# Kernel tuning notes

Measured on AMD Instinct MI355X. Metric: run time of the kernel, lower is better.

The kernel has to match this reference:

```python
import jax, jax.numpy as jnp
import numpy as np

S = 8192
Q_PARAM = 256
V_PARAM = 256
SCALE = 1.0 / np.sqrt(float(Q_PARAM)).astype(np.float32)


def setup_inputs() -> dict:
    key = jax.random.key(0)
    ks = jax.random.split(key, 12)
    init = lambda k, shape, fan_in: jax.random.uniform(k, shape, jnp.float32, -1.0, 1.0) / np.sqrt(float(fan_in))
    return {
        "query": jax.random.normal(ks[0], (S, Q_PARAM), jnp.float32),
        "key": jax.random.normal(ks[1], (S, Q_PARAM), jnp.float32),
        "value": jax.random.normal(ks[2], (S, V_PARAM), jnp.float32),
        "mask": jax.random.uniform(ks[3], (S, S), jnp.float32),
        "Wq": init(ks[4], (Q_PARAM, Q_PARAM), Q_PARAM),
        "bq": init(ks[5], (Q_PARAM,), Q_PARAM),
        "Wk": init(ks[6], (Q_PARAM, Q_PARAM), Q_PARAM),
        "bk": init(ks[7], (Q_PARAM,), Q_PARAM),
        "Wv": init(ks[8], (V_PARAM, V_PARAM), V_PARAM),
        "bv": init(ks[9], (V_PARAM,), V_PARAM),
        "Wo": init(ks[10], (V_PARAM, V_PARAM), V_PARAM),
        "bo": init(ks[11], (V_PARAM,), V_PARAM),
    }


def reference(query, key, value, mask, Wq, bq, Wk, bk, Wv, bv, Wo, bo):
    # torch nn.Linear: y = x @ W.T + b
    q = query @ Wq.T + bq          # [S, q]
    k = key @ Wk.T + bk            # [S, q]
    v = value @ Wv.T + bv          # [S, v]
    scores = q @ k.T               # [S, S]
    masked = scores * mask         # multiplicative mask BEFORE softmax
    h = jax.nn.softmax(masked * SCALE, axis=1)
    h = h @ v                      # [S, v]
    return h @ Wo.T + bo
```

## Files before the change

kernel.cpp:

```cpp
#include <hip/hip_runtime.h>


#define S 8192
#define NSPLIT 8
#define BM 128
#define BN 32
#define KSPL (S / NSPLIT)
#define NT (KSPL / BN)

typedef unsigned short ushort_t;
typedef __attribute__((ext_vector_type(8))) __bf16 bf16x8;
typedef __attribute__((ext_vector_type(4))) float f32x4;
typedef __attribute__((ext_vector_type(4))) ushort_t ushort4_t;
typedef __attribute__((ext_vector_type(8))) ushort_t ushort8_t;
typedef __attribute__((ext_vector_type(4))) unsigned uint4_t;

typedef const __attribute__((address_space(1))) unsigned int* gas_u32;
typedef __attribute__((address_space(3))) unsigned int* las_u32;

__device__ __forceinline__ ushort_t f2bf(float f) {
  unsigned u = __builtin_bit_cast(unsigned, f);
  u += 0x7FFFu + ((u >> 16) & 1u);
  return (ushort_t)(u >> 16);
}

__device__ __forceinline__ bf16x8 pack8(f32x4 a, f32x4 b) {
  ushort8_t u;
  u[0] = f2bf(a[0]); u[1] = f2bf(a[1]); u[2] = f2bf(a[2]); u[3] = f2bf(a[3]);
  u[4] = f2bf(b[0]); u[5] = f2bf(b[1]); u[6] = f2bf(b[2]); u[7] = f2bf(b[3]);
  return __builtin_bit_cast(bf16x8, u);
}

__device__ __forceinline__ unsigned cvt_pk_bf16(float lo, float hi) {
  unsigned r;
  asm("v_cvt_pk_bf16_f32 %0, %1, %2" : "=v"(r) : "v"(lo), "v"(hi));
  return r;
}

__global__ __launch_bounds__(256) void wconv_kernel(
    const float* __restrict__ w0, const float* __restrict__ w1,
    const float* __restrict__ w2, const float* __restrict__ w3,
    ushort_t* __restrict__ o0, ushort_t* __restrict__ o1,
    ushort_t* __restrict__ o2, ushort_t* __restrict__ o3) {
  const int m = blockIdx.y;
  const float* w = (m == 0) ? w0 : (m == 1) ? w1 : (m == 2) ? w2 : w3;
  ushort_t* o = (m == 0) ? o0 : (m == 1) ? o1 : (m == 2) ? o2 : o3;
  const int idx = (blockIdx.x * 256 + threadIdx.x) * 4;
  f32x4 v = *(const f32x4*)(w + idx);
  ushort4_t p;
  p[0] = f2bf(v[0]); p[1] = f2bf(v[1]); p[2] = f2bf(v[2]); p[3] = f2bf(v[3]);
  *(ushort4_t*)(o + idx) = p;
}

__global__ __launch_bounds__(256) void qkv_kernel(
    const float* __restrict__ query, const float* __restrict__ key,
    const float* __restrict__ value,
    const ushort_t* __restrict__ Wqb, const ushort_t* __restrict__ Wkb,
    const ushort_t* __restrict__ Wvb,
    const float* __restrict__ bq, const float* __restrict__ bk,
    const float* __restrict__ bv,
    ushort_t* __restrict__ qo, ushort_t* __restrict__ ko,
    ushort_t* __restrict__ vto) {
  __shared__ __align__(16) ushort_t tb[64 * 68];
  const int z = blockIdx.z;
  const float* inp = (z == 0) ? query : (z == 1) ? key : value;
  const ushort_t* Wb = (z == 0) ? Wqb : (z == 1) ? Wkb : Wvb;
  const float* bias = (z == 0) ? bq : (z == 1) ? bk : bv;

  const int tid = threadIdx.x;
  const int lane = tid & 63;
  const int w = tid >> 6;
  const int lr = lane & 15, lg = lane >> 4;
  const int brow0 = blockIdx.x * 64;
  const int row0 = brow0 + w * 16;
  const int col0 = blockIdx.y * 64;

  f32x4 acc[4] = {};
  const int arow = row0 + lr;
  const int kb = lg * 8;

  bf16x8 af[8];
#pragma unroll
  for (int ks = 0; ks < 8; ++ks) {
    const float* ap = inp + (size_t)arow * 256 + ks * 32 + kb;
    af[ks] = pack8(*(const f32x4*)ap, *(const f32x4*)(ap + 4));
  }
#pragma unroll
  for (int ks = 0; ks < 8; ++ks) {
#pragma unroll
    for (int n = 0; n < 4; ++n) {
      bf16x8 bb = *(const bf16x8*)(Wb + (size_t)(col0 + 16 * n + lr) * 256 + ks * 32 + kb);
      acc[n] = __builtin_amdgcn_mfma_f32_16x16x32_bf16(af[ks], bb, acc[n], 0, 0, 0);
    }
  }

  if (z < 2) {
    ushort_t* o = z ? ko : qo;
#pragma unroll
    for (int n = 0; n < 4; ++n) {
      const int col = col0 + 16 * n + lr;
      const float bv_ = bias[col];
      const int rbase = row0 + lg * 4;
#pragma unroll
      for (int r = 0; r < 4; ++r)
        o[(size_t)(rbase + r) * 256 + col] = f2bf(acc[n][r] + bv_);
    }
  } else {
#pragma unroll
    for (int n = 0; n < 4; ++n) {
      const int col = col0 + 16 * n + lr;
      const float bv_ = bias[col];
      const int cl = 16 * n + lr;
      const int rowl = w * 16 + lg * 4;
      ushort4_t pk;
#pragma unroll
      for (int r = 0; r < 4; ++r) pk[r] = f2bf(acc[n][r] + bv_);
      *(ushort4_t*)&tb[cl * 68 + rowl] = pk;
    }
    __syncthreads();
#pragma unroll
    for (int i = 0; i < 4; ++i) {
      int chunk = i * 256 + tid;
      int c = chunk >> 4;
      int off = (chunk & 15) * 4;
      ushort4_t v0 = *(const ushort4_t*)&tb[c * 68 + off];
      *(ushort4_t*)(vto + (size_t)(col0 + c) * S + brow0 + off) = v0;
    }
  }
}

__global__ __launch_bounds__(256) void oproj_kernel(const ushort_t* __restrict__ inp,
                                                    const ushort_t* __restrict__ Wb,
                                                    const float* __restrict__ bias,
                                                    float* __restrict__ outp) {
  const int tid = threadIdx.x;
  const int lane = tid & 63;
  const int w = tid >> 6;
  const int lr = lane & 15, lg = lane >> 4;
  const int row0 = blockIdx.x * 64 + w * 16;
  const int col0 = blockIdx.y * 64;

  f32x4 acc[4] = {};
  const int arow = row0 + lr;
  const int kb = lg * 8;
#pragma unroll
  for (int ks = 0; ks < 8; ++ks) {
    bf16x8 a = *(const bf16x8*)(inp + (size_t)arow * 256 + ks * 32 + kb);
#pragma unroll
    for (int n = 0; n < 4; ++n) {
      bf16x8 bb = *(const bf16x8*)(Wb + (size_t)(col0 + 16 * n + lr) * 256 + ks * 32 + kb);
      acc[n] = __builtin_amdgcn_mfma_f32_16x16x32_bf16(a, bb, acc[n], 0, 0, 0);
    }
  }
#pragma unroll
  for (int n = 0; n < 4; ++n) {
    const int col = col0 + 16 * n + lr;
    const float bv = bias[col];
    const int rbase = row0 + lg * 4;
#pragma unroll
    for (int r = 0; r < 4; ++r)
      outp[(size_t)(rbase + r) * 256 + col] = acc[n][r] + bv;
  }
}

__global__ __launch_bounds__(256, 2) void flash_kernel(
    const ushort_t* __restrict__ qg, const ushort_t* __restrict__ kbm,
    const ushort_t* __restrict__ vtb, const float* __restrict__ mask,
    float* __restrict__ Opart, float* __restrict__ lpart) {
  __shared__ __align__(16) ushort_t kt[2][BN * 256];
  __shared__ __align__(16) ushort_t vt[2][256 * BN];

  const int tid = threadIdx.x;
  const int lane = tid & 63;
  const int w = tid >> 6;
  const int lr = lane & 15, lg = lane >> 4;
  const int b = blockIdx.x;
  const int split = b & 7;
  const int qx = b >> 3;
  const int kvbase = split * KSPL;
  const int qrow0 = qx * BM + w * 32;

  bf16x8 qf[2][8];
#pragma unroll
  for (int qb = 0; qb < 2; ++qb)
#pragma unroll
    for (int ks = 0; ks < 8; ++ks)
      qf[qb][ks] = *(const bf16x8*)(qg + (size_t)(qrow0 + qb * 16 + lr) * 256 + ks * 32 + lg * 8);

  const float* mrow[2];
#pragma unroll
  for (int qb = 0; qb < 2; ++qb)
    mrow[qb] = mask + (size_t)(qrow0 + qb * 16 + lr) * S + lg * 4;

  f32x4 oacc[2][16] = {};
  float lsum[2] = {0.f, 0.f};
  const int vt_swz = ((lg ^ (lr & 3)) << 4);

  auto stage = [&](int bi, int kv0) {
#pragma unroll
    for (int it = 0; it < 4; ++it) {
      int chunk = it * 256 + (w << 6) + lane;
      int r = chunk >> 5;
      int c = (chunk & 31) ^ (r & 7);
      const ushort_t* src = kbm + (size_t)(kv0 + r) * 256 + c * 8;
      __builtin_amdgcn_global_load_lds((gas_u32)src,
                                       (las_u32)(&kt[bi][0] + it * 2048 + w * 512), 16, 0, 0);
    }
#pragma unroll
    for (int it = 0; it < 4; ++it) {
      int chunk = it * 256 + (w << 6) + lane;
      int r = chunk >> 2;
      int c = (chunk & 3) ^ (r & 3);
      const ushort_t* src = vtb + (size_t)r * S + kv0 + c * 8;
      __builtin_amdgcn_global_load_lds((gas_u32)src,
                                       (las_u32)(&vt[bi][0] + it * 2048 + w * 512), 16, 0, 0);
    }
  };

  f32x4 mcur[2][2];
  auto ld_mask = [&](int kv0) {
#pragma unroll
    for (int qb = 0; qb < 2; ++qb)
#pragma unroll
      for (int kb = 0; kb < 2; ++kb)
        mcur[qb][kb] = __builtin_nontemporal_load((const f32x4*)(mrow[qb] + kv0 + kb * 16));
  };

  stage(0, kvbase);
  ld_mask(kvbase);
  asm volatile("s_waitcnt vmcnt(4)" ::: "memory");
  __builtin_amdgcn_s_barrier();
  __builtin_amdgcn_sched_barrier(0);

  for (int t = 0; t < NT; ++t) {
    const int cur = t & 1;
    const int kvn = kvbase + ((t + 1 < NT) ? (t + 1) : t) * BN;

    stage(cur ^ 1, kvn);

    f32x4 sacc[2][2] = {};
    __builtin_amdgcn_s_setprio(1);
#pragma unroll
    for (int ks = 0; ks < 8; ++ks)
#pragma unroll
      for (int kb = 0; kb < 2; ++kb) {
        int addr = ((kb * 16 + lr) << 9) + ((((ks << 2) + lg) ^ (lr & 7)) << 4);
        bf16x8 kf = *(const bf16x8*)((const char*)&kt[cur][0] + addr);
        sacc[0][kb] = __builtin_amdgcn_mfma_f32_16x16x32_bf16(kf, qf[0][ks], sacc[0][kb], 0, 0, 0);
        sacc[1][kb] = __builtin_amdgcn_mfma_f32_16x16x32_bf16(kf, qf[1][ks], sacc[1][kb], 0, 0, 0);
      }
    __builtin_amdgcn_s_setprio(0);

    unsigned pw[2][2][2];
#pragma unroll
    for (int qb = 0; qb < 2; ++qb) {
      float p[8];
#pragma unroll
      for (int kb = 0; kb < 2; ++kb)
#pragma unroll
        for (int r = 0; r < 4; ++r) {
          float pv = __builtin_amdgcn_exp2f(sacc[qb][kb][r] * (mcur[qb][kb][r] * 0.09016844005556021f));
          p[kb * 4 + r] = pv;
          lsum[qb] += pv;
        }
      pw[qb][0][0] = cvt_pk_bf16(p[0], p[1]);
      pw[qb][0][1] = cvt_pk_bf16(p[2], p[3]);
      pw[qb][1][0] = cvt_pk_bf16(p[4], p[5]);
      pw[qb][1][1] = cvt_pk_bf16(p[6], p[7]);
    }

    ld_mask(kvn);

    bf16x8 pfrag[2];
#pragma unroll
    for (int qb = 0; qb < 2; ++qb) {
      unsigned a0 = pw[qb][0][0], a1 = pw[qb][0][1];
      unsigned b0 = pw[qb][1][0], b1 = pw[qb][1][1];
      asm("v_permlane32_swap_b32 %0, %1" : "+v"(a0), "+v"(b0));
      asm("v_permlane16_swap_b32 %0, %1" : "+v"(a0), "+v"(b0));
      asm("v_permlane32_swap_b32 %0, %1" : "+v"(a1), "+v"(b1));
      asm("v_permlane16_swap_b32 %0, %1" : "+v"(a1), "+v"(b1));
      uint4_t u = {a0, a1, b0, b1};
      pfrag[qb] = __builtin_bit_cast(bf16x8, u);
    }

    __builtin_amdgcn_s_setprio(1);
#pragma unroll
    for (int nd = 0; nd < 16; ++nd) {
      bf16x8 va = *(const bf16x8*)((const char*)&vt[cur][0] + nd * 1024 + lr * 64 + vt_swz);
      oacc[0][nd] = __builtin_amdgcn_mfma_f32_16x16x32_bf16(va, pfrag[0], oacc[0][nd], 0, 0, 0);
      oacc[1][nd] = __builtin_amdgcn_mfma_f32_16x16x32_bf16(va, pfrag[1], oacc[1][nd], 0, 0, 0);
    }
    __builtin_amdgcn_s_setprio(0);

    asm volatile("s_waitcnt vmcnt(4)" ::: "memory");
    __builtin_amdgcn_s_barrier();
    __builtin_amdgcn_sched_barrier(0);
  }

#pragma unroll
  for (int qb = 0; qb < 2; ++qb) {
    float v = lsum[qb];
    v += __shfl_xor(v, 16);
    v += __shfl_xor(v, 32);
    if (lane < 16)
      lpart[(size_t)split * S + qrow0 + qb * 16 + lr] = v;
#pragma unroll
    for (int nd = 0; nd < 16; ++nd)
      *(f32x4*)(Opart + ((size_t)split * S + qrow0 + qb * 16 + lr) * 256 + nd * 16 + lg * 4) = oacc[qb][nd];
  }
}

__global__ __launch_bounds__(256) void combine_kernel(const float* __restrict__ Opart,
                                                      const float* __restrict__ lpart,
                                                      ushort_t* __restrict__ hb) {
  const size_t idx = ((size_t)blockIdx.x * 256 + threadIdx.x) * 4;
  const int row = (int)(idx >> 8);
  float L = 0.f;
  f32x4 acc = {};
#pragma unroll
  for (int s2 = 0; s2 < NSPLIT; ++s2) {
    L += lpart[(size_t)s2 * S + row];
    f32x4 v = *(const f32x4*)(Opart + (size_t)s2 * S * 256 + idx);
    acc[0] += v[0]; acc[1] += v[1]; acc[2] += v[2]; acc[3] += v[3];
  }
  const float inv = 1.0f / L;
  ushort4_t p;
  p[0] = f2bf(acc[0] * inv); p[1] = f2bf(acc[1] * inv);
  p[2] = f2bf(acc[2] * inv); p[3] = f2bf(acc[3] * inv);
  *(ushort4_t*)(hb + idx) = p;
}

extern "C" void kernel_launch(void* const* d_in, const int* in_sizes, int n_in,
                              void* d_out, int out_size, void* d_ws, size_t ws_size,
                              hipStream_t stream) {
  const float* query = (const float*)d_in[0];
  const float* key   = (const float*)d_in[1];
  const float* value = (const float*)d_in[2];
  const float* mask  = (const float*)d_in[3];
  const float* Wq = (const float*)d_in[4];
  const float* bq = (const float*)d_in[5];
  const float* Wk = (const float*)d_in[6];
  const float* bk = (const float*)d_in[7];
  const float* Wv = (const float*)d_in[8];
  const float* bv = (const float*)d_in[9];
  const float* Wo = (const float*)d_in[10];
  const float* bo = (const float*)d_in[11];

  char* ws = (char*)d_ws;
  ushort_t* qb  = (ushort_t*)(ws);
  ushort_t* kb  = (ushort_t*)(ws + ((size_t)4  << 20));
  ushort_t* vtb = (ushort_t*)(ws + ((size_t)8  << 20));
  ushort_t* hb  = (ushort_t*)(ws + ((size_t)12 << 20));
  ushort_t* Wqb = (ushort_t*)(ws + ((size_t)16 << 20));
  ushort_t* Wkb = (ushort_t*)(ws + ((size_t)16 << 20) + (128u << 10));
  ushort_t* Wvb = (ushort_t*)(ws + ((size_t)16 << 20) + (256u << 10));
  ushort_t* Wob = (ushort_t*)(ws + ((size_t)16 << 20) + (384u << 10));
  float* lpart  = (float*)(ws + ((size_t)16 << 20) + (512u << 10));
  float* Opart  = (float*)(ws + ((size_t)17 << 20));

  wconv_kernel<<<dim3(64, 4), 256, 0, stream>>>(Wq, Wk, Wv, Wo, Wqb, Wkb, Wvb, Wob);

  qkv_kernel<<<dim3(S / 64, 4, 3), 256, 0, stream>>>(query, key, value,
                                                     Wqb, Wkb, Wvb, bq, bk, bv,
                                                     qb, kb, vtb);

  flash_kernel<<<dim3(512), 256, 0, stream>>>(qb, kb, vtb, mask, Opart, lpart);

  combine_kernel<<<dim3(S * 256 / 1024), 256, 0, stream>>>(Opart, lpart, hb);

  oproj_kernel<<<dim3(S / 64, 4), 256, 0, stream>>>(hb, Wob, bo, (float*)d_out);
}
```

Baseline: 226.6 us.

## Software-pipeline PV matmul one tile behind QK with triple-buffered V

```diff
diff --git a/kernel.cpp b/kernel.cpp
--- a/kernel.cpp
+++ b/kernel.cpp
@@ -168,7 +168,7 @@
     const ushort_t* __restrict__ vtb, const float* __restrict__ mask,
     float* __restrict__ Opart, float* __restrict__ lpart) {
   __shared__ __align__(16) ushort_t kt[2][BN * 256];
-  __shared__ __align__(16) ushort_t vt[2][256 * BN];
+  __shared__ __align__(16) ushort_t vt[3][256 * BN];
 
   const int tid = threadIdx.x;
   const int lane = tid & 63;
@@ -196,7 +196,14 @@
   float lsum[2] = {0.f, 0.f};
   const int vt_swz = ((lg ^ (lr & 3)) << 4);
 
-  auto stage = [&](int bi, int kv0) {
+  bf16x8 pfrag[2];
+  {
+    uint4_t z = {0u, 0u, 0u, 0u};
+    pfrag[0] = __builtin_bit_cast(bf16x8, z);
+    pfrag[1] = __builtin_bit_cast(bf16x8, z);
+  }
+
+  auto stage_k = [&](int bi, int kv0) {
 #pragma unroll
     for (int it = 0; it < 4; ++it) {
       int chunk = it * 256 + (w << 6) + lane;
@@ -206,6 +213,8 @@
       __builtin_amdgcn_global_load_lds((gas_u32)src,
                                        (las_u32)(&kt[bi][0] + it * 2048 + w * 512), 16, 0, 0);
     }
+  };
+  auto stage_v = [&](int bi, int kv0) {
 #pragma unroll
     for (int it = 0; it < 4; ++it) {
       int chunk = it * 256 + (w << 6) + lane;
@@ -226,26 +235,42 @@
         mcur[qb][kb] = __builtin_nontemporal_load((const f32x4*)(mrow[qb] + kv0 + kb * 16));
   };
 
-  stage(0, kvbase);
+  stage_k(0, kvbase);
+  stage_v(0, kvbase);
+  stage_v(2, kvbase);
+  __builtin_amdgcn_sched_barrier(0);
   ld_mask(kvbase);
   asm volatile("s_waitcnt vmcnt(4)" ::: "memory");
   __builtin_amdgcn_s_barrier();
   __builtin_amdgcn_sched_barrier(0);
 
+  int v_rd = 2, v_cu = 0, v_st = 1;
+
+#pragma unroll 1
   for (int t = 0; t < NT; ++t) {
-    const int cur = t & 1;
-    const int kvn = kvbase + ((t + 1 < NT) ? (t + 1) : t) * BN;
-
-    stage(cur ^ 1, kvn);
+    const int kcur = t & 1;
+    const int kvn = kvbase + ((t + 1 < NT) ? (t + 1) : 0) * BN;
+
+    stage_k(kcur ^ 1, kvn);
+    stage_v(v_st, kvn);
+    __builtin_amdgcn_sched_barrier(0);
+
+    const char* vbase = (const char*)&vt[0][0] + v_rd * 16384;
+    __builtin_amdgcn_s_setprio(1);
+#pragma unroll
+    for (int nd = 0; nd < 16; ++nd) {
+      bf16x8 va = *(const bf16x8*)(vbase + nd * 1024 + lr * 64 + vt_swz);
+      oacc[0][nd] = __builtin_amdgcn_mfma_f32_16x16x32_bf16(va, pfrag[0], oacc[0][nd], 0, 0, 0);
+      oacc[1][nd] = __builtin_amdgcn_mfma_f32_16x16x32_bf16(va, pfrag[1], oacc[1][nd], 0, 0, 0);
+    }
 
     f32x4 sacc[2][2] = {};
-    __builtin_amdgcn_s_setprio(1);
 #pragma unroll
     for (int ks = 0; ks < 8; ++ks)
 #pragma unroll
       for (int kb = 0; kb < 2; ++kb) {
         int addr = ((kb * 16 + lr) << 9) + ((((ks << 2) + lg) ^ (lr & 7)) << 4);
-        bf16x8 kf = *(const bf16x8*)((const char*)&kt[cur][0] + addr);
+        bf16x8 kf = *(const bf16x8*)((const char*)&kt[kcur][0] + addr);
         sacc[0][kb] = __builtin_amdgcn_mfma_f32_16x16x32_bf16(kf, qf[0][ks], sacc[0][kb], 0, 0, 0);
         sacc[1][kb] = __builtin_amdgcn_mfma_f32_16x16x32_bf16(kf, qf[1][ks], sacc[1][kb], 0, 0, 0);
       }
@@ -271,7 +296,6 @@
 
     ld_mask(kvn);
 
-    bf16x8 pfrag[2];
 #pragma unroll
     for (int qb = 0; qb < 2; ++qb) {
       unsigned a0 = pw[qb][0][0], a1 = pw[qb][0][1];
@@ -284,18 +308,23 @@
       pfrag[qb] = __builtin_bit_cast(bf16x8, u);
     }
 
-    __builtin_amdgcn_s_setprio(1);
-#pragma unroll
-    for (int nd = 0; nd < 16; ++nd) {
-      bf16x8 va = *(const bf16x8*)((const char*)&vt[cur][0] + nd * 1024 + lr * 64 + vt_swz);
-      oacc[0][nd] = __builtin_amdgcn_mfma_f32_16x16x32_bf16(va, pfrag[0], oacc[0][nd], 0, 0, 0);
-      oacc[1][nd] = __builtin_amdgcn_mfma_f32_16x16x32_bf16(va, pfrag[1], oacc[1][nd], 0, 0, 0);
-    }
-    __builtin_amdgcn_s_setprio(0);
-
     asm volatile("s_waitcnt vmcnt(4)" ::: "memory");
     __builtin_amdgcn_s_barrier();
     __builtin_amdgcn_sched_barrier(0);
+
+    int tmp = v_rd; v_rd = v_cu; v_cu = v_st; v_st = tmp;
+  }
+
+  {
+    const char* vbase = (const char*)&vt[0][0] + v_rd * 16384;
+    __builtin_amdgcn_s_setprio(1);
+#pragma unroll
+    for (int nd = 0; nd < 16; ++nd) {
+      bf16x8 va = *(const bf16x8*)(vbase + nd * 1024 + lr * 64 + vt_swz);
+      oacc[0][nd] = __builtin_amdgcn_mfma_f32_16x16x32_bf16(va, pfrag[0], oacc[0][nd], 0, 0, 0);
+      oacc[1][nd] = __builtin_amdgcn_mfma_f32_16x16x32_bf16(va, pfrag[1], oacc[1][nd], 0, 0, 0);
+    }
+    __builtin_amdgcn_s_setprio(0);
   }
 
 #pragma unroll
```

After: 237.5 us. 1.05x slower.

## Use 8 waves per flash block with 16 query rows each instead of 32

Applied to the files above, without the earlier changes.

```diff
diff --git a/kernel.cpp b/kernel.cpp
--- a/kernel.cpp
+++ b/kernel.cpp
@@ -163,7 +163,7 @@
   }
 }
 
-__global__ __launch_bounds__(256, 2) void flash_kernel(
+__global__ __launch_bounds__(512, 1) void flash_kernel(
     const ushort_t* __restrict__ qg, const ushort_t* __restrict__ kbm,
     const ushort_t* __restrict__ vtb, const float* __restrict__ mask,
     float* __restrict__ Opart, float* __restrict__ lpart) {
@@ -178,67 +178,54 @@
   const int split = b & 7;
   const int qx = b >> 3;
   const int kvbase = split * KSPL;
-  const int qrow0 = qx * BM + w * 32;
-
-  bf16x8 qf[2][8];
-#pragma unroll
-  for (int qb = 0; qb < 2; ++qb)
-#pragma unroll
-    for (int ks = 0; ks < 8; ++ks)
-      qf[qb][ks] = *(const bf16x8*)(qg + (size_t)(qrow0 + qb * 16 + lr) * 256 + ks * 32 + lg * 8);
-
-  const float* mrow[2];
-#pragma unroll
-  for (int qb = 0; qb < 2; ++qb)
-    mrow[qb] = mask + (size_t)(qrow0 + qb * 16 + lr) * S + lg * 4;
-
-  f32x4 oacc[2][16] = {};
-  float lsum[2] = {0.f, 0.f};
-  const int vt_swz = ((lg ^ (lr & 3)) << 4);
+  const int qrow0 = qx * BM + w * 16;
+
+  bf16x8 qf[8];
+#pragma unroll
+  for (int ks = 0; ks < 8; ++ks)
+    qf[ks] = *(const bf16x8*)(qg + (size_t)(qrow0 + lr) * 256 + ks * 32 + lg * 8);
+
+  const float* mrow = mask + (size_t)(qrow0 + lr) * S + lg * 4;
+
+  f32x4 oacc[16] = {};
+  float lsum = 0.f;
+  const int vt_swz = ((lg ^ ((lr >> 1) & 3)) << 4);
 
   auto stage = [&](int bi, int kv0) {
 #pragma unroll
-    for (int it = 0; it < 4; ++it) {
-      int chunk = it * 256 + (w << 6) + lane;
+    for (int it = 0; it < 2; ++it) {
+      int chunk = it * 512 + tid;
       int r = chunk >> 5;
       int c = (chunk & 31) ^ (r & 7);
       const ushort_t* src = kbm + (size_t)(kv0 + r) * 256 + c * 8;
       __builtin_amdgcn_global_load_lds((gas_u32)src,
-                                       (las_u32)(&kt[bi][0] + it * 2048 + w * 512), 16, 0, 0);
-    }
-#pragma unroll
-    for (int it = 0; it < 4; ++it) {
-      int chunk = it * 256 + (w << 6) + lane;
+                                       (las_u32)(&kt[bi][0] + chunk * 8), 16, 0, 0);
+    }
+#pragma unroll
+    for (int it = 0; it < 2; ++it) {
+      int chunk = it * 512 + tid;
       int r = chunk >> 2;
-      int c = (chunk & 3) ^ (r & 3);
+      int c = (chunk & 3) ^ ((r >> 1) & 3);
       const ushort_t* src = vtb + (size_t)r * S + kv0 + c * 8;
       __builtin_amdgcn_global_load_lds((gas_u32)src,
-                                       (las_u32)(&vt[bi][0] + it * 2048 + w * 512), 16, 0, 0);
+                                       (las_u32)(&vt[bi][0] + chunk * 8), 16, 0, 0);
     }
   };
 
-  f32x4 mcur[2][2];
-  auto ld_mask = [&](int kv0) {
-#pragma unroll
-    for (int qb = 0; qb < 2; ++qb)
-#pragma unroll
-      for (int kb = 0; kb < 2; ++kb)
-        mcur[qb][kb] = __builtin_nontemporal_load((const f32x4*)(mrow[qb] + kv0 + kb * 16));
-  };
-
   stage(0, kvbase);
-  ld_mask(kvbase);
-  asm volatile("s_waitcnt vmcnt(4)" ::: "memory");
+  asm volatile("s_waitcnt vmcnt(0)" ::: "memory");
   __builtin_amdgcn_s_barrier();
   __builtin_amdgcn_sched_barrier(0);
 
   for (int t = 0; t < NT; ++t) {
     const int cur = t & 1;
+    const int kv0 = kvbase + t * BN;
     const int kvn = kvbase + ((t + 1 < NT) ? (t + 1) : t) * BN;
 
     stage(cur ^ 1, kvn);
-
-    f32x4 sacc[2][2] = {};
+    __builtin_amdgcn_sched_barrier(0);
+
+    f32x4 sacc[2] = {};
     __builtin_amdgcn_s_setprio(1);
 #pragma unroll
     for (int ks = 0; ks < 8; ++ks)
@@ -246,69 +233,56 @@
       for (int kb = 0; kb < 2; ++kb) {
         int addr = ((kb * 16 + lr) << 9) + ((((ks << 2) + lg) ^ (lr & 7)) << 4);
         bf16x8 kf = *(const bf16x8*)((const char*)&kt[cur][0] + addr);
-        sacc[0][kb] = __builtin_amdgcn_mfma_f32_16x16x32_bf16(kf, qf[0][ks], sacc[0][kb], 0, 0, 0);
-        sacc[1][kb] = __builtin_amdgcn_mfma_f32_16x16x32_bf16(kf, qf[1][ks], sacc[1][kb], 0, 0, 0);
+        sacc[kb] = __builtin_amdgcn_mfma_f32_16x16x32_bf16(kf, qf[ks], sacc[kb], 0, 0, 0);
       }
     __builtin_amdgcn_s_setprio(0);
 
-    unsigned pw[2][2][2];
-#pragma unroll
-    for (int qb = 0; qb < 2; ++qb) {
-      float p[8];
-#pragma unroll
-      for (int kb = 0; kb < 2; ++kb)
-#pragma unroll
-        for (int r = 0; r < 4; ++r) {
-          float pv = __builtin_amdgcn_exp2f(sacc[qb][kb][r] * (mcur[qb][kb][r] * 0.09016844005556021f));
-          p[kb * 4 + r] = pv;
-          lsum[qb] += pv;
-        }
-      pw[qb][0][0] = cvt_pk_bf16(p[0], p[1]);
-      pw[qb][0][1] = cvt_pk_bf16(p[2], p[3]);
-      pw[qb][1][0] = cvt_pk_bf16(p[4], p[5]);
-      pw[qb][1][1] = cvt_pk_bf16(p[6], p[7]);
-    }
-
-    ld_mask(kvn);
-
-    bf16x8 pfrag[2];
-#pragma unroll
-    for (int qb = 0; qb < 2; ++qb) {
-      unsigned a0 = pw[qb][0][0], a1 = pw[qb][0][1];
-      unsigned b0 = pw[qb][1][0], b1 = pw[qb][1][1];
-      asm("v_permlane32_swap_b32 %0, %1" : "+v"(a0), "+v"(b0));
-      asm("v_permlane16_swap_b32 %0, %1" : "+v"(a0), "+v"(b0));
-      asm("v_permlane32_swap_b32 %0, %1" : "+v"(a1), "+v"(b1));
-      asm("v_permlane16_swap_b32 %0, %1" : "+v"(a1), "+v"(b1));
-      uint4_t u = {a0, a1, b0, b1};
-      pfrag[qb] = __builtin_bit_cast(bf16x8, u);
-    }
+    float p[8];
+#pragma unroll
+    for (int kb = 0; kb < 2; ++kb) {
+      f32x4 mv = __builtin_nontemporal_load((const f32x4*)(mrow + kv0 + kb * 16));
+#pragma unroll
+      for (int r = 0; r < 4; ++r) {
+        float pv = __builtin_amdgcn_exp2f(sacc[kb][r] * (mv[r] * 0.09016844005556021f));
+        p[kb * 4 + r] = pv;
+        lsum += pv;
+      }
+    }
+    unsigned pw0 = cvt_pk_bf16(p[0], p[1]);
+    unsigned pw1 = cvt_pk_bf16(p[2], p[3]);
+    unsigned pw2 = cvt_pk_bf16(p[4], p[5]);
+    unsigned pw3 = cvt_pk_bf16(p[6], p[7]);
+
+    asm("v_permlane32_swap_b32 %0, %1" : "+v"(pw0), "+v"(pw2));
+    asm("v_permlane16_swap_b32 %0, %1" : "+v"(pw0), "+v"(pw2));
+    asm("v_permlane32_swap_b32 %0, %1" : "+v"(pw1), "+v"(pw3));
+    asm("v_permlane16_swap_b32 %0, %1" : "+v"(pw1), "+v"(pw3));
+    uint4_t u = {pw0, pw1, pw2, pw3};
+    bf16x8 pfrag = __builtin_bit_cast(bf16x8, u);
 
     __builtin_amdgcn_s_setprio(1);
 #pragma unroll
     for (int nd = 0; nd < 16; ++nd) {
       bf16x8 va = *(const bf16x8*)((const char*)&vt[cur][0] + nd * 1024 + lr * 64 + vt_swz);
-      oacc[0][nd] = __builtin_amdgcn_mfma_f32_16x16x32_bf16(va, pfrag[0], oacc[0][nd], 0, 0, 0);
-      oacc[1][nd] = __builtin_amdgcn_mfma_f32_16x16x32_bf16(va, pfrag[1], oacc[1][nd], 0, 0, 0);
+      oacc[nd] = __builtin_amdgcn_mfma_f32_16x16x32_bf16(va, pfrag, oacc[nd], 0, 0, 0);
     }
     __builtin_amdgcn_s_setprio(0);
 
-    asm volatile("s_waitcnt vmcnt(4)" ::: "memory");
+    asm volatile("s_waitcnt vmcnt(0)" ::: "memory");
     __builtin_amdgcn_s_barrier();
     __builtin_amdgcn_sched_barrier(0);
   }
 
-#pragma unroll
-  for (int qb = 0; qb < 2; ++qb) {
-    float v = lsum[qb];
+  {
+    float v = lsum;
     v += __shfl_xor(v, 16);
     v += __shfl_xor(v, 32);
     if (lane < 16)
-      lpart[(size_t)split * S + qrow0 + qb * 16 + lr] = v;
-#pragma unroll
-    for (int nd = 0; nd < 16; ++nd)
-      *(f32x4*)(Opart + ((size_t)split * S + qrow0 + qb * 16 + lr) * 256 + nd * 16 + lg * 4) = oacc[qb][nd];
-  }
+      lpart[(size_t)split * S + qrow0 + lr] = v;
+  }
+#pragma unroll
+  for (int nd = 0; nd < 16; ++nd)
+    *(f32x4*)(Opart + ((size_t)split * S + qrow0 + lr) * 256 + nd * 16 + lg * 4) = oacc[nd];
 }
 
 __global__ __launch_bounds__(256) void combine_kernel(const float* __restrict__ Opart,
@@ -365,7 +339,7 @@
                                                      Wqb, Wkb, Wvb, bq, bk, bv,
                                                      qb, kb, vtb);
 
-  flash_kernel<<<dim3(512), 256, 0, stream>>>(qb, kb, vtb, mask, Opart, lpart);
+  flash_kernel<<<dim3(512), 512, 0, stream>>>(qb, kb, vtb, mask, Opart, lpart);
 
   combine_kernel<<<dim3(S * 256 / 1024), 256, 0, stream>>>(Opart, lpart, hb);
 
```

New measurement: 231.0 us. No clear change (+1.9%).

## Load K and V fragments directly from global memory instead of LDS staging

Applied to the files above, without the earlier changes.

```diff
diff --git a/kernel.cpp b/kernel.cpp
--- a/kernel.cpp
+++ b/kernel.cpp
@@ -7,6 +7,7 @@
 #define BN 32
 #define KSPL (S / NSPLIT)
 #define NT (KSPL / BN)
+#define VSTRIDE 8224
 
 typedef unsigned short ushort_t;
 typedef __attribute__((ext_vector_type(8))) __bf16 bf16x8;
@@ -14,9 +15,6 @@
 typedef __attribute__((ext_vector_type(4))) ushort_t ushort4_t;
 typedef __attribute__((ext_vector_type(8))) ushort_t ushort8_t;
 typedef __attribute__((ext_vector_type(4))) unsigned uint4_t;
-
-typedef const __attribute__((address_space(1))) unsigned int* gas_u32;
-typedef __attribute__((address_space(3))) unsigned int* las_u32;
 
 __device__ __forceinline__ ushort_t f2bf(float f) {
   unsigned u = __builtin_bit_cast(unsigned, f);
@@ -124,7 +122,7 @@
       int c = chunk >> 4;
       int off = (chunk & 15) * 4;
       ushort4_t v0 = *(const ushort4_t*)&tb[c * 68 + off];
-      *(ushort4_t*)(vto + (size_t)(col0 + c) * S + brow0 + off) = v0;
+      *(ushort4_t*)(vto + (size_t)(col0 + c) * VSTRIDE + brow0 + off) = v0;
     }
   }
 }
@@ -163,13 +161,10 @@
   }
 }
 
-__global__ __launch_bounds__(256, 2) void flash_kernel(
+__global__ __launch_bounds__(256, 1) void flash_kernel(
     const ushort_t* __restrict__ qg, const ushort_t* __restrict__ kbm,
     const ushort_t* __restrict__ vtb, const float* __restrict__ mask,
     float* __restrict__ Opart, float* __restrict__ lpart) {
-  __shared__ __align__(16) ushort_t kt[2][BN * 256];
-  __shared__ __align__(16) ushort_t vt[2][256 * BN];
-
   const int tid = threadIdx.x;
   const int lane = tid & 63;
   const int w = tid >> 6;
@@ -194,64 +189,39 @@
 
   f32x4 oacc[2][16] = {};
   float lsum[2] = {0.f, 0.f};
-  const int vt_swz = ((lg ^ (lr & 3)) << 4);
-
-  auto stage = [&](int bi, int kv0) {
-#pragma unroll
-    for (int it = 0; it < 4; ++it) {
-      int chunk = it * 256 + (w << 6) + lane;
-      int r = chunk >> 5;
-      int c = (chunk & 31) ^ (r & 7);
-      const ushort_t* src = kbm + (size_t)(kv0 + r) * 256 + c * 8;
-      __builtin_amdgcn_global_load_lds((gas_u32)src,
-                                       (las_u32)(&kt[bi][0] + it * 2048 + w * 512), 16, 0, 0);
-    }
-#pragma unroll
-    for (int it = 0; it < 4; ++it) {
-      int chunk = it * 256 + (w << 6) + lane;
-      int r = chunk >> 2;
-      int c = (chunk & 3) ^ (r & 3);
-      const ushort_t* src = vtb + (size_t)r * S + kv0 + c * 8;
-      __builtin_amdgcn_global_load_lds((gas_u32)src,
-                                       (las_u32)(&vt[bi][0] + it * 2048 + w * 512), 16, 0, 0);
-    }
-  };
 
   f32x4 mcur[2][2];
-  auto ld_mask = [&](int kv0) {
-#pragma unroll
-    for (int qb = 0; qb < 2; ++qb)
-#pragma unroll
-      for (int kb = 0; kb < 2; ++kb)
-        mcur[qb][kb] = __builtin_nontemporal_load((const f32x4*)(mrow[qb] + kv0 + kb * 16));
-  };
-
-  stage(0, kvbase);
-  ld_mask(kvbase);
-  asm volatile("s_waitcnt vmcnt(4)" ::: "memory");
-  __builtin_amdgcn_s_barrier();
-  __builtin_amdgcn_sched_barrier(0);
-
+#pragma unroll
+  for (int qb = 0; qb < 2; ++qb)
+#pragma unroll
+    for (int kb = 0; kb < 2; ++kb)
+      mcur[qb][kb] = __builtin_nontemporal_load((const f32x4*)(mrow[qb] + kvbase + kb * 16));
+
+#pragma unroll 1
   for (int t = 0; t < NT; ++t) {
-    const int cur = t & 1;
+    const int kv0 = kvbase + t * BN;
     const int kvn = kvbase + ((t + 1 < NT) ? (t + 1) : t) * BN;
 
-    stage(cur ^ 1, kvn);
+    bf16x8 vfA[8];
+#pragma unroll
+    for (int nd = 0; nd < 8; ++nd)
+      vfA[nd] = *(const bf16x8*)(vtb + (size_t)(nd * 16 + lr) * VSTRIDE + kv0 + lg * 8);
 
     f32x4 sacc[2][2] = {};
     __builtin_amdgcn_s_setprio(1);
 #pragma unroll
-    for (int ks = 0; ks < 8; ++ks)
-#pragma unroll
-      for (int kb = 0; kb < 2; ++kb) {
-        int addr = ((kb * 16 + lr) << 9) + ((((ks << 2) + lg) ^ (lr & 7)) << 4);
-        bf16x8 kf = *(const bf16x8*)((const char*)&kt[cur][0] + addr);
-        sacc[0][kb] = __builtin_amdgcn_mfma_f32_16x16x32_bf16(kf, qf[0][ks], sacc[0][kb], 0, 0, 0);
-        sacc[1][kb] = __builtin_amdgcn_mfma_f32_16x16x32_bf16(kf, qf[1][ks], sacc[1][kb], 0, 0, 0);
-      }
+    for (int ks = 0; ks < 8; ++ks) {
+      const size_t koff = (size_t)(kv0 + lr) * 256 + ks * 32 + lg * 8;
+      bf16x8 kf0 = *(const bf16x8*)(kbm + koff);
+      bf16x8 kf1 = *(const bf16x8*)(kbm + koff + 16 * 256);
+      sacc[0][0] = __builtin_amdgcn_mfma_f32_16x16x32_bf16(kf0, qf[0][ks], sacc[0][0], 0, 0, 0);
+      sacc[1][0] = __builtin_amdgcn_mfma_f32_16x16x32_bf16(kf0, qf[1][ks], sacc[1][0], 0, 0, 0);
+      sacc[0][1] = __builtin_amdgcn_mfma_f32_16x16x32_bf16(kf1, qf[0][ks], sacc[0][1], 0, 0, 0);
+      sacc[1][1] = __builtin_amdgcn_mfma_f32_16x16x32_bf16(kf1, qf[1][ks], sacc[1][1], 0, 0, 0);
+    }
     __builtin_amdgcn_s_setprio(0);
 
-    unsigned pw[2][2][2];
+    unsigned pw[2][4];
 #pragma unroll
     for (int qb = 0; qb < 2; ++qb) {
       float p[8];
@@ -263,19 +233,23 @@
           p[kb * 4 + r] = pv;
           lsum[qb] += pv;
         }
-      pw[qb][0][0] = cvt_pk_bf16(p[0], p[1]);
-      pw[qb][0][1] = cvt_pk_bf16(p[2], p[3]);
-      pw[qb][1][0] = cvt_pk_bf16(p[4], p[5]);
-      pw[qb][1][1] = cvt_pk_bf16(p[6], p[7]);
-    }
-
-    ld_mask(kvn);
+      pw[qb][0] = cvt_pk_bf16(p[0], p[1]);
+      pw[qb][1] = cvt_pk_bf16(p[2], p[3]);
+      pw[qb][2] = cvt_pk_bf16(p[4], p[5]);
+      pw[qb][3] = cvt_pk_bf16(p[6], p[7]);
+    }
+
+#pragma unroll
+    for (int qb = 0; qb < 2; ++qb)
+#pragma unroll
+      for (int kb = 0; kb < 2; ++kb)
+        mcur[qb][kb] = __builtin_nontemporal_load((const f32x4*)(mrow[qb] + kvn + kb * 16));
 
     bf16x8 pfrag[2];
 #pragma unroll
     for (int qb = 0; qb < 2; ++qb) {
-      unsigned a0 = pw[qb][0][0], a1 = pw[qb][0][1];
-      unsigned b0 = pw[qb][1][0], b1 = pw[qb][1][1];
+      unsigned a0 = pw[qb][0], a1 = pw[qb][1];
+      unsigned b0 = pw[qb][2], b1 = pw[qb][3];
       asm("v_permlane32_swap_b32 %0, %1" : "+v"(a0), "+v"(b0));
       asm("v_permlane16_swap_b32 %0, %1" : "+v"(a0), "+v"(b0));
       asm("v_permlane32_swap_b32 %0, %1" : "+v"(a1), "+v"(b1));
@@ -284,18 +258,23 @@
       pfrag[qb] = __builtin_bit_cast(bf16x8, u);
     }
 
+    bf16x8 vfB[8];
+#pragma unroll
+    for (int nd = 0; nd < 8; ++nd)
+      vfB[nd] = *(const bf16x8*)(vtb + (size_t)((nd + 8) * 16 + lr) * VSTRIDE + kv0 + lg * 8);
+
     __builtin_amdgcn_s_setprio(1);
 #pragma unroll
-    for (int nd = 0; nd < 16; ++nd) {
-      bf16x8 va = *(const bf16x8*)((const char*)&vt[cur][0] + nd * 1024 + lr * 64 + vt_swz);
-      oacc[0][nd] = __builtin_amdgcn_mfma_f32_16x16x32_bf16(va, pfrag[0], oacc[0][nd], 0, 0, 0);
-      oacc[1][nd] = __builtin_amdgcn_mfma_f32_16x16x32_bf16(va, pfrag[1], oacc[1][nd], 0, 0, 0);
+    for (int nd = 0; nd < 8; ++nd) {
+      oacc[0][nd] = __builtin_amdgcn_mfma_f32_16x16x32_bf16(vfA[nd], pfrag[0], oacc[0][nd], 0, 0, 0);
+      oacc[1][nd] = __builtin_amdgcn_mfma_f32_16x16x32_bf16(vfA[nd], pfrag[1], oacc[1][nd], 0, 0, 0);
+    }
+#pragma unroll
+    for (int nd = 0; nd < 8; ++nd) {
+      oacc[0][nd + 8] = __builtin_amdgcn_mfma_f32_16x16x32_bf16(vfB[nd], pfrag[0], oacc[0][nd + 8], 0, 0, 0);
+      oacc[1][nd + 8] = __builtin_amdgcn_mfma_f32_16x16x32_bf16(vfB[nd], pfrag[1], oacc[1][nd + 8], 0, 0, 0);
     }
     __builtin_amdgcn_s_setprio(0);
-
-    asm volatile("s_waitcnt vmcnt(4)" ::: "memory");
-    __builtin_amdgcn_s_barrier();
-    __builtin_amdgcn_sched_barrier(0);
   }
 
 #pragma unroll
@@ -351,13 +330,13 @@
   ushort_t* qb  = (ushort_t*)(ws);
   ushort_t* kb  = (ushort_t*)(ws + ((size_t)4  << 20));
   ushort_t* vtb = (ushort_t*)(ws + ((size_t)8  << 20));
-  ushort_t* hb  = (ushort_t*)(ws + ((size_t)12 << 20));
-  ushort_t* Wqb = (ushort_t*)(ws + ((size_t)16 << 20));
-  ushort_t* Wkb = (ushort_t*)(ws + ((size_t)16 << 20) + (128u << 10));
-  ushort_t* Wvb = (ushort_t*)(ws + ((size_t)16 << 20) + (256u << 10));
-  ushort_t* Wob = (ushort_t*)(ws + ((size_t)16 << 20) + (384u << 10));
-  float* lpart  = (float*)(ws + ((size_t)16 << 20) + (512u << 10));
-  float* Opart  = (float*)(ws + ((size_t)17 << 20));
+  ushort_t* hb  = (ushort_t*)(ws + ((size_t)13 << 20));
+  ushort_t* Wqb = (ushort_t*)(ws + ((size_t)17 << 20));
+  ushort_t* Wkb = (ushort_t*)(ws + ((size_t)17 << 20) + (128u << 10));
+  ushort_t* Wvb = (ushort_t*)(ws + ((size_t)17 << 20) + (256u << 10));
+  ushort_t* Wob = (ushort_t*)(ws + ((size_t)17 << 20) + (384u << 10));
+  float* lpart  = (float*)(ws + ((size_t)17 << 20) + (512u << 10));
+  float* Opart  = (float*)(ws + ((size_t)18 << 20));
 
   wconv_kernel<<<dim3(64, 4), 256, 0, stream>>>(Wq, Wk, Wv, Wo, Wqb, Wkb, Wvb, Wob);
 
```

Measured after the change: 433.0 us. +91.1%, slower.
